# Optimization experiments

Measured on AMD Instinct MI355X. Metric: run time of the kernel, lower is better.

Reference implementation:

```python
import jax, jax.numpy as jnp
import numpy as np

GAMMA = 0.00390625  # 1/256

def _rbf_mean(x, y):
    # mean of exp(-gamma * ||x_i - y_j||^2) via GEMM expansion (no NxMxD intermediate)
    x2 = jnp.sum(x * x, axis=1)              # [N]
    y2 = jnp.sum(y * y, axis=1)              # [M]
    d2 = x2[:, None] + y2[None, :] - 2.0 * (x @ y.T)   # [N, M]
    d2 = jnp.maximum(d2, 0.0)
    return jnp.mean(jnp.exp(-GAMMA * d2))

def setup_inputs() -> dict:
    key = jax.random.key(0)
    k1, k2 = jax.random.split(key)
    z_s = jax.random.normal(k1, (8192, 256), dtype=jnp.float32)
    z_t = jax.random.normal(k2, (8192, 256), dtype=jnp.float32)
    return {"z_s": z_s, "z_t": z_t}

def reference(z_s, z_t):
    return _rbf_mean(z_s, z_s) + _rbf_mean(z_t, z_t) - 2.0 * _rbf_mean(z_s, z_t)
```

## Files before the change

kernel.cpp:

```cpp
#include <hip/hip_runtime.h>

#define NH   8192
#define DIM  256
#define NTOT 16384
#define TM   256
#define TN   128
#define NRB  64
#define NTILES 4160
#define FCUM(R) ((R) * (129 - (R)))

constexpr float GAMMA = 0.00390625f;
constexpr float QSCL  = 6.0f / 127.0f;

using short4v = __attribute__((ext_vector_type(4))) short;
using i32x4   = __attribute__((ext_vector_type(4))) int;
using f32x4   = __attribute__((ext_vector_type(4))) float;

__global__ void prep_kernel(const float* __restrict__ zs,
                            const float* __restrict__ zt,
                            signed char* __restrict__ Zq,
                            float* __restrict__ n2) {
    int w = threadIdx.x >> 6, l = threadIdx.x & 63;
    int row = blockIdx.x * 4 + w;
    const float* zp = (row < NH) ? zs + (size_t)row * DIM
                                 : zt + (size_t)(row - NH) * DIM;
    float4 v = *(const float4*)(zp + l * 4);
    float s = v.x * v.x + v.y * v.y + v.z * v.z + v.w * v.w;
#pragma unroll
    for (int off = 32; off; off >>= 1) s += __shfl_xor(s, off);
    if (l == 0) n2[row] = s;

    const float inv = 127.0f / 6.0f;
    float x[4] = {v.x, v.y, v.z, v.w};
    int pk = 0;
#pragma unroll
    for (int j = 0; j < 4; ++j) {
        int q = (int)rintf(fminf(fmaxf(x[j] * inv, -127.0f), 127.0f));
        pk |= (q & 0xFF) << (8 * j);
    }
    *(int*)(Zq + (size_t)row * DIM + l * 4) = pk;
}

__global__ __launch_bounds__(256, 2)
void mmd_mfma_kernel(const signed char* __restrict__ Zq,
                     const float* __restrict__ n2,
                     double* __restrict__ partial) {
    __shared__ __align__(16) unsigned char lds[3][24576];

    const int tid = threadIdx.x;
    const int w = tid >> 6, l = tid & 63;
    const int wr = w >> 1, wc = w & 1;
    const int fr = l & 15;
    const int g  = l >> 4;

    int t = ((int)blockIdx.x & 7) * (NTILES / 8) + ((int)blockIdx.x >> 3);

    int R = (int)((129.0 - sqrt(129.0 * 129.0 - 4.0 * (double)t)) * 0.5);
    if (R < 0) R = 0;
    if (R > NRB - 1) R = NRB - 1;
    while (R < NRB - 1 && FCUM(R + 1) <= t) ++R;
    while (R > 0 && FCUM(R) > t) --R;
    const int C = 2 * R + (t - FCUM(R));
    const int xbase = R * TM, ybase = C * TN;
    const bool straddle = (C <= 2 * R + 1);

    const signed char* gA = Zq + (size_t)xbase * DIM;
    const signed char* gB = Zq + (size_t)ybase * DIM;

    const int slotp = g ^ ((fr >> 1) & 3);
    const int aoff = (wr * 128 + fr) * 64 + slotp * 16;
    const int boff = 16384 + (wc * 64 + fr) * 64 + slotp * 16;

    i32x4 acc[8][4];
#pragma unroll
    for (int m = 0; m < 8; ++m)
#pragma unroll
        for (int n = 0; n < 4; ++n) acc[m][n] = {0, 0, 0, 0};

#define STAGE(KCB, P)                                                                \
    {                                                                                \
        _Pragma("unroll")                                                            \
        for (int q = 0; q < 4; ++q) {                             \
            const int idx = q * 256 + tid;                                           \
            const int row = idx >> 2;                                                \
            const int slot = (idx & 3) ^ ((row >> 1) & 3);                           \
            const signed char* src = gA + (size_t)row * DIM + (KCB) + slot * 16;     \
            __builtin_amdgcn_global_load_lds(src, &lds[P][idx * 16], 16, 0, 0);      \
        }                                                                            \
        _Pragma("unroll")                                                            \
        for (int q = 0; q < 2; ++q) {                              \
            const int idx = q * 256 + tid;                                           \
            const int row = idx >> 2;                                                \
            const int slot = (idx & 3) ^ ((row >> 1) & 3);                           \
            const signed char* src = gB + (size_t)row * DIM + (KCB) + slot * 16;     \
            __builtin_amdgcn_global_load_lds(src, &lds[P][16384 + idx * 16], 16, 0, 0);\
        }                                                                            \
    }

    STAGE(0, 0);
    STAGE(64, 1);

#pragma unroll
    for (int ch = 0; ch < 4; ++ch) {
        const int p = ch % 3;
        if (ch < 2) {
            STAGE((ch + 2) * 64, (ch + 2) % 3);
            asm volatile("s_waitcnt vmcnt(12)" ::: "memory");
        } else if (ch == 2) {
            asm volatile("s_waitcnt vmcnt(6)" ::: "memory");
        } else {
            asm volatile("s_waitcnt vmcnt(0)" ::: "memory");
        }
        __builtin_amdgcn_s_barrier();

        i32x4 bq[4];
#pragma unroll
        for (int n = 0; n < 4; ++n) bq[n] = *(const i32x4*)&lds[p][boff + n * 1024];
        __builtin_amdgcn_s_setprio(1);
#pragma unroll
        for (int m = 0; m < 8; ++m) {
            i32x4 aq = *(const i32x4*)&lds[p][aoff + m * 1024];
#pragma unroll
            for (int n = 0; n < 4; ++n)
                acc[m][n] = __builtin_amdgcn_mfma_i32_16x16x64_i8(aq, bq[n], acc[m][n], 0, 0, 0);
        }
        __builtin_amdgcn_s_setprio(0);
        __builtin_amdgcn_s_barrier();
    }

    const float GL  = GAMMA * 1.4426950408889634f;
    const float K2i = 2.0f * GL * QSCL * QSCL;
    float ncy[4];
    int   gjs[4];
#pragma unroll
    for (int n = 0; n < 4; ++n) {
        gjs[n] = ybase + wc * 64 + n * 16 + fr;
        ncy[n] = -GL * n2[gjs[n]];
    }
    float fsum;
    if (!straddle) {
        float fs0 = 0.f, fs1 = 0.f, fs2 = 0.f, fs3 = 0.f;
#pragma unroll
        for (int m = 0; m < 8; ++m) {
#pragma unroll
            for (int j = 0; j < 4; ++j) {
                float cx = GL * n2[xbase + wr * 128 + m * 16 + g * 4 + j];
                fs0 += __builtin_amdgcn_exp2f(fmaf(K2i, (float)acc[m][0][j], ncy[0]) - cx);
                fs1 += __builtin_amdgcn_exp2f(fmaf(K2i, (float)acc[m][1][j], ncy[1]) - cx);
                fs2 += __builtin_amdgcn_exp2f(fmaf(K2i, (float)acc[m][2][j], ncy[2]) - cx);
                fs3 += __builtin_amdgcn_exp2f(fmaf(K2i, (float)acc[m][3][j], ncy[3]) - cx);
            }
        }
        fsum = ((fs0 + fs1) + (fs2 + fs3)) * 2.0f;
    } else {
        fsum = 0.f;
#pragma unroll
        for (int m = 0; m < 8; ++m) {
#pragma unroll
            for (int j = 0; j < 4; ++j) {
                const int gi = xbase + wr * 128 + m * 16 + g * 4 + j;
                float cx = GL * n2[gi];
#pragma unroll
                for (int n = 0; n < 4; ++n) {
                    float e = __builtin_amdgcn_exp2f(fmaf(K2i, (float)acc[m][n][j], ncy[n]) - cx);
                    float wgt = (gi < gjs[n]) ? 2.0f : ((gi == gjs[n]) ? 1.0f : 0.0f);
                    fsum += wgt * e;
                }
            }
        }
    }

#pragma unroll
    for (int off = 32; off; off >>= 1) fsum += __shfl_xor(fsum, off);

    __syncthreads();
    double* wsum = (double*)&lds[0][0];
    if (l == 0) wsum[w] = (double)fsum;
    __syncthreads();
    if (tid == 0) {
        double tot = wsum[0] + wsum[1] + wsum[2] + wsum[3];
        double sgn = ((xbase < NH) == (ybase < NH)) ? 1.0 : -1.0;
        partial[blockIdx.x] = sgn * tot;
    }
}

__global__ void reduce_partials_kernel(const double* __restrict__ partial,
                                       float* __restrict__ out) {
    __shared__ double ws[4];
    double s = 0.0;
    for (int i = threadIdx.x; i < NTILES; i += 256) s += partial[i];
#pragma unroll
    for (int off = 32; off; off >>= 1) s += __shfl_xor(s, off);
    if ((threadIdx.x & 63) == 0) ws[threadIdx.x >> 6] = s;
    __syncthreads();
    if (threadIdx.x == 0) {
        double tot = ws[0] + ws[1] + ws[2] + ws[3];
        out[0] = (float)(tot / ((double)NH * (double)NH));
    }
}

extern "C" void kernel_launch(void* const* d_in, const int* in_sizes, int n_in,
                              void* d_out, int out_size, void* d_ws, size_t ws_size,
                              hipStream_t stream) {
    const float* zs = (const float*)d_in[0];
    const float* zt = (const float*)d_in[1];
    float* out = (float*)d_out;

    signed char* Zq = (signed char*)d_ws;
    float*  n2      = (float*)((char*)d_ws + 4194304);
    double* partial = (double*)((char*)d_ws + 4259840);

    prep_kernel<<<NTOT / 4, 256, 0, stream>>>(zs, zt, Zq, n2);
    mmd_mfma_kernel<<<NTILES, 256, 0, stream>>>(Zq, n2, partial);
    reduce_partials_kernel<<<1, 256, 0, stream>>>(partial, out);
}
```

Measured before the change: 69.70 us.

## Stage full-K A tile in LDS once, stream B fragments from global

```diff
diff --git a/kernel.cpp b/kernel.cpp
--- a/kernel.cpp
+++ b/kernel.cpp
@@ -12,9 +12,8 @@
 constexpr float GAMMA = 0.00390625f;
 constexpr float QSCL  = 6.0f / 127.0f;
 
-using short4v = __attribute__((ext_vector_type(4))) short;
-using i32x4   = __attribute__((ext_vector_type(4))) int;
-using f32x4   = __attribute__((ext_vector_type(4))) float;
+using i32x4 = __attribute__((ext_vector_type(4))) int;
+using f32x4 = __attribute__((ext_vector_type(4))) float;
 
 __global__ void prep_kernel(const float* __restrict__ zs,
                             const float* __restrict__ zt,
@@ -45,7 +44,7 @@
 void mmd_mfma_kernel(const signed char* __restrict__ Zq,
                      const float* __restrict__ n2,
                      double* __restrict__ partial) {
-    __shared__ __align__(16) unsigned char lds[3][24576];
+    __shared__ __align__(16) unsigned char lds[65536];
 
     const int tid = threadIdx.x;
     const int w = tid >> 6, l = tid & 63;
@@ -69,7 +68,11 @@
 
     const int slotp = g ^ ((fr >> 1) & 3);
     const int aoff = (wr * 128 + fr) * 64 + slotp * 16;
-    const int boff = 16384 + (wc * 64 + fr) * 64 + slotp * 16;
+
+    const signed char* gBr[4];
+#pragma unroll
+    for (int n = 0; n < 4; ++n)
+        gBr[n] = gB + (size_t)(wc * 64 + n * 16 + fr) * DIM + g * 16;
 
     i32x4 acc[8][4];
 #pragma unroll
@@ -77,56 +80,52 @@
 #pragma unroll
         for (int n = 0; n < 4; ++n) acc[m][n] = {0, 0, 0, 0};
 
-#define STAGE(KCB, P)                                                                \
-    {                                                                                \
-        _Pragma("unroll")                                                            \
-        for (int q = 0; q < 4; ++q) {                             \
-            const int idx = q * 256 + tid;                                           \
-            const int row = idx >> 2;                                                \
-            const int slot = (idx & 3) ^ ((row >> 1) & 3);                           \
-            const signed char* src = gA + (size_t)row * DIM + (KCB) + slot * 16;     \
-            __builtin_amdgcn_global_load_lds(src, &lds[P][idx * 16], 16, 0, 0);      \
-        }                                                                            \
-        _Pragma("unroll")                                                            \
-        for (int q = 0; q < 2; ++q) {                              \
-            const int idx = q * 256 + tid;                                           \
-            const int row = idx >> 2;                                                \
-            const int slot = (idx & 3) ^ ((row >> 1) & 3);                           \
-            const signed char* src = gB + (size_t)row * DIM + (KCB) + slot * 16;     \
-            __builtin_amdgcn_global_load_lds(src, &lds[P][16384 + idx * 16], 16, 0, 0);\
-        }                                                                            \
-    }
-
-    STAGE(0, 0);
-    STAGE(64, 1);
-
 #pragma unroll
     for (int ch = 0; ch < 4; ++ch) {
-        const int p = ch % 3;
-        if (ch < 2) {
-            STAGE((ch + 2) * 64, (ch + 2) % 3);
-            asm volatile("s_waitcnt vmcnt(12)" ::: "memory");
-        } else if (ch == 2) {
-            asm volatile("s_waitcnt vmcnt(6)" ::: "memory");
-        } else {
-            asm volatile("s_waitcnt vmcnt(0)" ::: "memory");
+#pragma unroll
+        for (int q = 0; q < 4; ++q) {
+            const int idx = q * 256 + tid;
+            const int row = idx >> 2;
+            const int slot = (idx & 3) ^ ((row >> 1) & 3);
+            const signed char* src = gA + (size_t)row * DIM + ch * 64 + slot * 16;
+            __builtin_amdgcn_global_load_lds(src, &lds[ch * 16384 + idx * 16], 16, 0, 0);
         }
-        __builtin_amdgcn_s_barrier();
-
-        i32x4 bq[4];
-#pragma unroll
-        for (int n = 0; n < 4; ++n) bq[n] = *(const i32x4*)&lds[p][boff + n * 1024];
-        __builtin_amdgcn_s_setprio(1);
-#pragma unroll
-        for (int m = 0; m < 8; ++m) {
-            i32x4 aq = *(const i32x4*)&lds[p][aoff + m * 1024];
-#pragma unroll
-            for (int n = 0; n < 4; ++n)
-                acc[m][n] = __builtin_amdgcn_mfma_i32_16x16x64_i8(aq, bq[n], acc[m][n], 0, 0, 0);
-        }
-        __builtin_amdgcn_s_setprio(0);
-        __builtin_amdgcn_s_barrier();
-    }
+    }
+    asm volatile("" ::: "memory");
+
+    i32x4 bqA[4], bqB[4];
+#pragma unroll
+    for (int n = 0; n < 4; ++n) bqA[n] = *(const i32x4*)(gBr[n] + 0 * 64);
+#pragma unroll
+    for (int n = 0; n < 4; ++n) bqB[n] = *(const i32x4*)(gBr[n] + 1 * 64);
+    asm volatile("" ::: "memory");
+
+    asm volatile("s_waitcnt vmcnt(8)" ::: "memory");
+    __builtin_amdgcn_s_barrier();
+
+#define CHUNK(CH, BQ, RELOAD)                                                         \
+    {                                                                                 \
+        __builtin_amdgcn_s_setprio(1);                                                \
+        _Pragma("unroll")                                                             \
+        for (int m = 0; m < 8; ++m) {                                                 \
+            i32x4 aq = *(const i32x4*)&lds[(CH) * 16384 + aoff + m * 1024];           \
+            _Pragma("unroll")                                                         \
+            for (int n = 0; n < 4; ++n)                                               \
+                acc[m][n] = __builtin_amdgcn_mfma_i32_16x16x64_i8(aq, BQ[n], acc[m][n], 0, 0, 0); \
+        }                                                                             \
+        __builtin_amdgcn_s_setprio(0);                                                \
+        RELOAD;                                                                       \
+    }
+#define RELB(BQ, CH)                                                                  \
+    {                                                                                 \
+        _Pragma("unroll")                                                             \
+        for (int n = 0; n < 4; ++n) BQ[n] = *(const i32x4*)(gBr[n] + (CH) * 64);      \
+    }
+
+    CHUNK(0, bqA, RELB(bqA, 2))
+    CHUNK(1, bqB, RELB(bqB, 3))
+    CHUNK(2, bqA, )
+    CHUNK(3, bqB, )
 
     const float GL  = GAMMA * 1.4426950408889634f;
     const float K2i = 2.0f * GL * QSCL * QSCL;
@@ -174,7 +173,7 @@
     for (int off = 32; off; off >>= 1) fsum += __shfl_xor(fsum, off);
 
     __syncthreads();
-    double* wsum = (double*)&lds[0][0];
+    double* wsum = (double*)&lds[0];
     if (l == 0) wsum[w] = (double)fsum;
     __syncthreads();
     if (tid == 0) {
```

New measurement: 78.80 us. 13.1% more time.
